# Performance work log

Hardware: AMD Instinct MI355X
Metric: run time of the kernel (lower is better)

Reference implementation:

```python
import jax, jax.numpy as jnp
import numpy as np

N = 1024
C_LOCAL = 384
C_PAIR = 128
HEADS = 8
KEY_SIZE = 32
LN_EPS = 1e-5


def setup_inputs() -> dict:
    key = jax.random.key(0)
    ks = jax.random.split(key, 5)
    local = jax.random.normal(ks[0], (N, C_LOCAL), dtype=jnp.float32)
    pair = jax.random.normal(ks[1], (N, N, C_PAIR), dtype=jnp.float32)
    mask = jnp.ones((N,), dtype=bool)
    ln_scale = jnp.ones((C_LOCAL,), dtype=jnp.float32)
    ln_offset = jnp.zeros((C_LOCAL,), dtype=jnp.float32)
    W_value = jax.random.normal(ks[2], (C_LOCAL, HEADS * KEY_SIZE), dtype=jnp.float32) * (1.0 / np.sqrt(C_LOCAL))
    W_attn = jax.random.normal(ks[3], (C_PAIR, HEADS), dtype=jnp.float32) * (1.0 / np.sqrt(C_PAIR))
    W_out = jax.random.normal(ks[4], (HEADS * KEY_SIZE, C_LOCAL), dtype=jnp.float32) * (1.0 / np.sqrt(HEADS * KEY_SIZE))
    return {"local": local, "pair": pair, "mask": mask,
            "ln_scale": ln_scale, "ln_offset": ln_offset,
            "W_value": W_value, "W_attn": W_attn, "W_out": W_out}


def reference(local, pair, mask, ln_scale, ln_offset, W_value, W_attn, W_out):
    # pair_mask[i, j] = mask[i] & mask[j]
    pair_mask = (mask[:, None] & mask[None, :])[..., None]  # [N, N, 1]

    # LayerNorm over last axis (create_scale=True, create_offset=True)
    mu = jnp.mean(local, axis=-1, keepdims=True)
    var = jnp.var(local, axis=-1, keepdims=True)
    local_ln = (local - mu) * jax.lax.rsqrt(var + LN_EPS) * ln_scale + ln_offset

    # value projection -> [N, heads, key_size]
    value = (local_ln @ W_value).reshape(local.shape[0], HEADS, KEY_SIZE)

    # pair-bias attention logits -> [N, N, heads]
    attn = pair @ W_attn
    attn = jnp.where(pair_mask, attn, -1e9)
    attn = jax.nn.softmax(attn, axis=1)
    attn = jnp.where(pair_mask, attn, 0.0)

    # weighted average over j, per head -> [N, heads, key_size] -> [N, heads*key_size]
    out = jnp.einsum('ijh,jhc->ihc', attn, value).reshape(local.shape[0], -1)
    return out @ W_out
```

## Files before the change

### kernel.cpp

```cpp
#include <hip/hip_runtime.h>
#include <cstddef>

#define NN 1024
#define CL 384
#define CP 128
#define NH 8
#define KS 32
#define HK 256
#define CHK 32
#define NCHK (NN/CHK)

typedef float floatx4 __attribute__((ext_vector_type(4)));

template<int CTRL>
__device__ __forceinline__ float dpp_mov(float v) {
    return __int_as_float(__builtin_amdgcn_update_dpp(
        0, __float_as_int(v), CTRL, 0xF, 0xF, true));
}

__device__ __forceinline__ float4 ntload4(const float* p) {
    floatx4 t = __builtin_nontemporal_load((const floatx4*)p);
    float4 r; r.x = t.x; r.y = t.y; r.z = t.z; r.w = t.w;
    return r;
}

__global__ __launch_bounds__(256) void k_ln_value(
    const float* __restrict__ local_, const float* __restrict__ ln_scale,
    const float* __restrict__ ln_offset, const float* __restrict__ Wv,
    float* __restrict__ value)
{
    __shared__ float ln_s[4][CL];
    const int tid = threadIdx.x;
    const int w = tid >> 6, lane = tid & 63;
    const int r = blockIdx.x * 4 + w;
    const float* lp = local_ + (size_t)r * CL;
    float x[6]; float s1 = 0.f, s2 = 0.f;
#pragma unroll
    for (int k = 0; k < 6; ++k) { x[k] = lp[lane + 64*k]; s1 += x[k]; s2 += x[k]*x[k]; }
#pragma unroll
    for (int m = 1; m < 64; m <<= 1) { s1 += __shfl_xor(s1, m); s2 += __shfl_xor(s2, m); }
    const float mean = s1 * (1.f/CL);
    const float var  = fmaxf(s2 * (1.f/CL) - mean*mean, 0.f);
    const float rstd = rsqrtf(var + 1e-5f);
#pragma unroll
    for (int k = 0; k < 6; ++k) {
        const int c = lane + 64*k;
        ln_s[w][c] = (x[k]-mean)*rstd*ln_scale[c] + ln_offset[c];
    }
    __syncthreads();
    const int m_ = tid;
    float acc0=0.f, acc1=0.f, acc2=0.f, acc3=0.f;
    for (int c0 = 0; c0 < CL; c0 += 8) {
        float wv[8];
#pragma unroll
        for (int cc = 0; cc < 8; ++cc) wv[cc] = Wv[(size_t)(c0+cc)*HK + m_];
        {
            const float4 a = *(const float4*)&ln_s[0][c0];
            const float4 b = *(const float4*)&ln_s[0][c0+4];
            acc0 += a.x*wv[0]+a.y*wv[1]+a.z*wv[2]+a.w*wv[3]+b.x*wv[4]+b.y*wv[5]+b.z*wv[6]+b.w*wv[7];
        }
        {
            const float4 a = *(const float4*)&ln_s[1][c0];
            const float4 b = *(const float4*)&ln_s[1][c0+4];
            acc1 += a.x*wv[0]+a.y*wv[1]+a.z*wv[2]+a.w*wv[3]+b.x*wv[4]+b.y*wv[5]+b.z*wv[6]+b.w*wv[7];
        }
        {
            const float4 a = *(const float4*)&ln_s[2][c0];
            const float4 b = *(const float4*)&ln_s[2][c0+4];
            acc2 += a.x*wv[0]+a.y*wv[1]+a.z*wv[2]+a.w*wv[3]+b.x*wv[4]+b.y*wv[5]+b.z*wv[6]+b.w*wv[7];
        }
        {
            const float4 a = *(const float4*)&ln_s[3][c0];
            const float4 b = *(const float4*)&ln_s[3][c0+4];
            acc3 += a.x*wv[0]+a.y*wv[1]+a.z*wv[2]+a.w*wv[3]+b.x*wv[4]+b.y*wv[5]+b.z*wv[6]+b.w*wv[7];
        }
    }
    const int rb = blockIdx.x*4;
    value[(size_t)(rb+0)*HK + m_] = acc0;
    value[(size_t)(rb+1)*HK + m_] = acc1;
    value[(size_t)(rb+2)*HK + m_] = acc2;
    value[(size_t)(rb+3)*HK + m_] = acc3;
}

__global__ __launch_bounds__(256, 4) void k_attn(
    const float* __restrict__ pair, const int* __restrict__ mask,
    const float* __restrict__ Wa, const float* __restrict__ value,
    const float* __restrict__ Wo, float* __restrict__ outp)
{
    __shared__ float zf[NN];
    __shared__ float ps[2][NH][CHK+4];
    __shared__ float sep[8*NH];
    __shared__ float ov4[4][64][4];
    __shared__ float ov[HK];

    const int tid = threadIdx.x;
    const int g = tid >> 5;
    const int sub5 = tid & 31;
    const int i = blockIdx.x;
    const bool bmi = mask[i] != 0;

    for (int k = tid; k < NN; k += 256)
        zf[k] = (bmi && (mask[k] != 0)) ? 1.f : 0.f;

    float wreg[32];
    {
        const float4* wp = (const float4*)(Wa + sub5*4*NH);
#pragma unroll
        for (int k = 0; k < 8; ++k) {
            const float4 t4 = wp[k];
            wreg[4*k+0]=t4.x; wreg[4*k+1]=t4.y; wreg[4*k+2]=t4.z; wreg[4*k+3]=t4.w;
        }
    }

    const int  myh   = (sub5 & 1)*4 + ((sub5 >> 1) & 1)*2 + ((sub5 >> 3) & 1);
    const bool owner = (sub5 & 0x14) == 0;

    const int q  = tid >> 6;
    const int mq = tid & 63;
    const int pvh = mq >> 3;
    float4 ac4; ac4.x = ac4.y = ac4.z = ac4.w = 0.f;
    float se_loc = 0.f;

    const float* pb = pair + (size_t)i*NN*CP + sub5*4;

    float4 dA[4], dB[4];

    auto PREFETCH = [&](float4* d, int jc) {
#pragma unroll
        for (int s = 0; s < 4; ++s)
            d[s] = ntload4(pb + (size_t)(jc + g*4 + s)*CP);
    };

    auto LOGITS = [&](const float4* d, int jc, int pbuf) {
#pragma unroll
        for (int s = 0; s < 4; ++s) {
            const float4 cur = d[s];
            float acc[8];
#pragma unroll
            for (int h = 0; h < 8; ++h)
                acc[h] = cur.x*wreg[h] + cur.y*wreg[8+h] + cur.z*wreg[16+h] + cur.w*wreg[24+h];
            const bool b0 = (sub5 & 1) != 0;
            const bool b1 = (sub5 & 2) != 0;
            const bool b3 = (sub5 & 8) != 0;
            float r4[4];
#pragma unroll
            for (int k = 0; k < 4; ++k)
                r4[k] = (b0 ? acc[k+4] : acc[k]) + dpp_mov<0xB1>(b0 ? acc[k] : acc[k+4]);
            float r2[2];
#pragma unroll
            for (int k = 0; k < 2; ++k)
                r2[k] = (b1 ? r4[k+2] : r4[k]) + dpp_mov<0x4E>(b1 ? r4[k] : r4[k+2]);
            float r1 = (b3 ? r2[1] : r2[0]) + dpp_mov<0x128>(b3 ? r2[0] : r2[1]);
            r1 += __shfl_xor(r1, 4);
            r1 += __shfl_xor(r1, 16);
            const int jj = g*4 + s;
            const float pt = zf[jc + jj] * __expf(r1);
            se_loc += pt;
            ps[pbuf][myh][jj] = pt;
        }
    };

    auto PV = [&](int jc, int pbuf) {
        const float* vb = value + (size_t)jc*HK + mq*4;
#pragma unroll
        for (int k = 0; k < 8; ++k) {
            const int jj = 4*k + q;
            const float p = ps[pbuf][pvh][jj];
            const float4 v4 = *(const float4*)(vb + (size_t)jj*HK);
            ac4.x += p*v4.x; ac4.y += p*v4.y; ac4.z += p*v4.z; ac4.w += p*v4.w;
        }
    };

    PREFETCH(dA, 0);
    PREFETCH(dB, CHK);
    __syncthreads();

    for (int it = 0; it < NCHK/2; ++it) {
        const int k0 = it*2;
        LOGITS(dA, k0*CHK, 0);
        if (k0 > 0) PV((k0-1)*CHK, 1);
        __builtin_amdgcn_sched_barrier(0);
        if (k0+2 < NCHK) PREFETCH(dA, (k0+2)*CHK);
        asm volatile("s_waitcnt lgkmcnt(0)" ::: "memory");
        __builtin_amdgcn_s_barrier();
        LOGITS(dB, (k0+1)*CHK, 1);
        PV(k0*CHK, 0);
        __builtin_amdgcn_sched_barrier(0);
        if (k0+3 < NCHK) PREFETCH(dB, (k0+3)*CHK);
        asm volatile("s_waitcnt lgkmcnt(0)" ::: "memory");
        __builtin_amdgcn_s_barrier();
    }
    PV((NCHK-1)*CHK, 1);

    if (owner) sep[g*NH + myh] = se_loc;
    ov4[q][mq][0] = ac4.x; ov4[q][mq][1] = ac4.y;
    ov4[q][mq][2] = ac4.z; ov4[q][mq][3] = ac4.w;
    __syncthreads();

    {
        const int m = tid;
        const float s4 = ov4[0][m>>2][m&3] + ov4[1][m>>2][m&3]
                       + ov4[2][m>>2][m&3] + ov4[3][m>>2][m&3];
        const int h = m >> 5;
        float se = 0.f;
#pragma unroll
        for (int k = 0; k < 8; ++k) se += sep[k*NH + h];
        const float inv = (se > 0.f) ? (1.f/se) : 0.f;
        ov[m] = s4 * inv;
    }
    __syncthreads();

    for (int o = tid; o < CL; o += 256) {
        float a0 = 0.f;
        for (int m = 0; m < HK; m += 4) {
            const float4 x0 = *(const float4*)&ov[m];
            a0 += x0.x*Wo[(size_t)(m+0)*CL + o] + x0.y*Wo[(size_t)(m+1)*CL + o]
                + x0.z*Wo[(size_t)(m+2)*CL + o] + x0.w*Wo[(size_t)(m+3)*CL + o];
        }
        outp[(size_t)i*CL + o] = a0;
    }
}

extern "C" void kernel_launch(void* const* d_in, const int* in_sizes, int n_in,
                              void* d_out, int out_size, void* d_ws, size_t ws_size,
                              hipStream_t stream)
{
    (void)in_sizes; (void)n_in; (void)out_size; (void)ws_size;
    const float* local_ = (const float*)d_in[0];
    const float* pair   = (const float*)d_in[1];
    const int*   mask   = (const int*)d_in[2];
    const float* scale  = (const float*)d_in[3];
    const float* offset = (const float*)d_in[4];
    const float* Wv     = (const float*)d_in[5];
    const float* Wa     = (const float*)d_in[6];
    const float* Wo     = (const float*)d_in[7];
    float* value = (float*)d_ws;
    k_ln_value<<<NN/4, 256, 0, stream>>>(local_, scale, offset, Wv, value);
    k_attn<<<NN, 256, 0, stream>>>(pair, mask, Wa, value, Wo, (float*)d_out);
}
```

Before: 164.5 us.

## Split key range across waves and exchange probabilities via shuffles instead of LDS barriers

Each wavefront now owns a contiguous quarter of the key dimension and computes logits, exp, and the P·V accumulation within the wave. Probabilities are broadcast with lane shuffles rather than staged through a shared-memory buffer, which removes the per-chunk block barriers and double-buffered LDS traffic. Register prefetch of the next pair rows is kept as a simple cur/next swap. The cost is more shuffle instructions and per-wave partial sums that must be reduced at the end, and the loop still prefetches a wrapped-around chunk on the last iteration.

```diff
diff --git a/kernel.cpp b/kernel.cpp
--- a/kernel.cpp
+++ b/kernel.cpp
@@ -7,8 +7,6 @@
 #define NH 8
 #define KS 32
 #define HK 256
-#define CHK 32
-#define NCHK (NN/CHK)
 
 typedef float floatx4 __attribute__((ext_vector_type(4)));
 
@@ -88,14 +86,15 @@
     const float* __restrict__ Wo, float* __restrict__ outp)
 {
     __shared__ float zf[NN];
-    __shared__ float ps[2][NH][CHK+4];
-    __shared__ float sep[8*NH];
+    __shared__ float sep[4][NH];
     __shared__ float ov4[4][64][4];
     __shared__ float ov[HK];
 
-    const int tid = threadIdx.x;
-    const int g = tid >> 5;
-    const int sub5 = tid & 31;
+    const int tid  = threadIdx.x;
+    const int w    = tid >> 6;
+    const int lane = tid & 63;
+    const int sub5 = lane & 31;
+    const int half = lane >> 5;
     const int i = blockIdx.x;
     const bool bmi = mask[i] != 0;
 
@@ -112,33 +111,37 @@
         }
     }
 
-    const int  myh   = (sub5 & 1)*4 + ((sub5 >> 1) & 1)*2 + ((sub5 >> 3) & 1);
-    const bool owner = (sub5 & 0x14) == 0;
-
-    const int q  = tid >> 6;
-    const int mq = tid & 63;
-    const int pvh = mq >> 3;
+    const int hpv  = lane >> 3;
+    const int srcE = ((hpv>>2)&1) + 2*((hpv>>1)&1) + 8*(hpv&1);
+    const int srcO = srcE + 32;
+
+    const int jbase = w * 256;
+    const float* pb = pair + (size_t)i*NN*CP + sub5*4;
+
     float4 ac4; ac4.x = ac4.y = ac4.z = ac4.w = 0.f;
     float se_loc = 0.f;
 
-    const float* pb = pair + (size_t)i*NN*CP + sub5*4;
-
-    float4 dA[4], dB[4];
-
-    auto PREFETCH = [&](float4* d, int jc) {
+    float4 cur[4], nxt[4];
+#pragma unroll
+    for (int s = 0; s < 4; ++s)
+        cur[s] = ntload4(pb + (size_t)(jbase + 2*s + half)*CP);
+
+    __syncthreads();
+
+    for (int t = 0; t < 32; ++t) {
+        const int j0 = jbase + t*8;
+        const int jp = jbase + (((t+1)&31)*8);
 #pragma unroll
         for (int s = 0; s < 4; ++s)
-            d[s] = ntload4(pb + (size_t)(jc + g*4 + s)*CP);
-    };
-
-    auto LOGITS = [&](const float4* d, int jc, int pbuf) {
+            nxt[s] = ntload4(pb + (size_t)(jp + 2*s + half)*CP);
+
 #pragma unroll
         for (int s = 0; s < 4; ++s) {
-            const float4 cur = d[s];
+            const float4 c = cur[s];
             float acc[8];
 #pragma unroll
             for (int h = 0; h < 8; ++h)
-                acc[h] = cur.x*wreg[h] + cur.y*wreg[8+h] + cur.z*wreg[16+h] + cur.w*wreg[24+h];
+                acc[h] = c.x*wreg[h] + c.y*wreg[8+h] + c.z*wreg[16+h] + c.w*wreg[24+h];
             const bool b0 = (sub5 & 1) != 0;
             const bool b1 = (sub5 & 2) != 0;
             const bool b3 = (sub5 & 8) != 0;
@@ -153,48 +156,25 @@
             float r1 = (b3 ? r2[1] : r2[0]) + dpp_mov<0x128>(b3 ? r2[0] : r2[1]);
             r1 += __shfl_xor(r1, 4);
             r1 += __shfl_xor(r1, 16);
-            const int jj = g*4 + s;
-            const float pt = zf[jc + jj] * __expf(r1);
-            se_loc += pt;
-            ps[pbuf][myh][jj] = pt;
-        }
-    };
-
-    auto PV = [&](int jc, int pbuf) {
-        const float* vb = value + (size_t)jc*HK + mq*4;
-#pragma unroll
-        for (int k = 0; k < 8; ++k) {
-            const int jj = 4*k + q;
-            const float p = ps[pbuf][pvh][jj];
-            const float4 v4 = *(const float4*)(vb + (size_t)jj*HK);
-            ac4.x += p*v4.x; ac4.y += p*v4.y; ac4.z += p*v4.z; ac4.w += p*v4.w;
-        }
-    };
-
-    PREFETCH(dA, 0);
-    PREFETCH(dB, CHK);
-    __syncthreads();
-
-    for (int it = 0; it < NCHK/2; ++it) {
-        const int k0 = it*2;
-        LOGITS(dA, k0*CHK, 0);
-        if (k0 > 0) PV((k0-1)*CHK, 1);
-        __builtin_amdgcn_sched_barrier(0);
-        if (k0+2 < NCHK) PREFETCH(dA, (k0+2)*CHK);
-        asm volatile("s_waitcnt lgkmcnt(0)" ::: "memory");
-        __builtin_amdgcn_s_barrier();
-        LOGITS(dB, (k0+1)*CHK, 1);
-        PV(k0*CHK, 0);
-        __builtin_amdgcn_sched_barrier(0);
-        if (k0+3 < NCHK) PREFETCH(dB, (k0+3)*CHK);
-        asm volatile("s_waitcnt lgkmcnt(0)" ::: "memory");
-        __builtin_amdgcn_s_barrier();
-    }
-    PV((NCHK-1)*CHK, 1);
-
-    if (owner) sep[g*NH + myh] = se_loc;
-    ov4[q][mq][0] = ac4.x; ov4[q][mq][1] = ac4.y;
-    ov4[q][mq][2] = ac4.z; ov4[q][mq][3] = ac4.w;
+            const float pe = __expf(r1);
+            const float p_e = __shfl(pe, srcE) * zf[j0 + 2*s];
+            const float p_o = __shfl(pe, srcO) * zf[j0 + 2*s + 1];
+            se_loc += p_e + p_o;
+            const float* vb = value + (size_t)(j0 + 2*s)*HK + lane*4;
+            const float4 ve = *(const float4*)vb;
+            const float4 vo = *(const float4*)(vb + HK);
+            ac4.x += p_e*ve.x + p_o*vo.x;
+            ac4.y += p_e*ve.y + p_o*vo.y;
+            ac4.z += p_e*ve.z + p_o*vo.z;
+            ac4.w += p_e*ve.w + p_o*vo.w;
+        }
+#pragma unroll
+        for (int s = 0; s < 4; ++s) cur[s] = nxt[s];
+    }
+
+    if ((lane & 7) == 0) sep[w][hpv] = se_loc;
+    ov4[w][lane][0] = ac4.x; ov4[w][lane][1] = ac4.y;
+    ov4[w][lane][2] = ac4.z; ov4[w][lane][3] = ac4.w;
     __syncthreads();
 
     {
@@ -202,9 +182,7 @@
         const float s4 = ov4[0][m>>2][m&3] + ov4[1][m>>2][m&3]
                        + ov4[2][m>>2][m&3] + ov4[3][m>>2][m&3];
         const int h = m >> 5;
-        float se = 0.f;
-#pragma unroll
-        for (int k = 0; k < 8; ++k) se += sep[k*NH + h];
+        const float se = sep[0][h] + sep[1][h] + sep[2][h] + sep[3][h];
         const float inv = (se > 0.f) ? (1.f/se) : 0.f;
         ov[m] = s4 * inv;
     }
```

After: 154.9 us. -5.8%, faster.
